# Optimization experiments

Hardware: AMD Instinct MI355X
Metric: run time of the kernel (lower is better)

## Reference

```python
import jax, jax.numpy as jnp
import numpy as np

NH, HD = 4, 16          # num_heads, head_dim (proj_dim = 64)
SCALE = HD ** -0.5
EPS = 1e-5
G = 16                  # GroupNorm groups = min(16, channels)


def _conv1x1(W, b, x):
    # 1x1 conv == channel-mixing matmul: W (out,in), x (B,in,H,W)
    return jnp.einsum('pc,bchw->bphw', W, x) + b[None, :, None, None]


def _attend(Wq, bq, Wk, bk, Wv, bv, Wo, bo, query, context):
    B, C, H, Wd = query.shape
    N = H * Wd
    q = _conv1x1(Wq, bq, query).astype(jnp.float32).reshape(B, NH, HD, N)
    k = _conv1x1(Wk, bk, context).astype(jnp.float32).reshape(B, NH, HD, N)
    v = _conv1x1(Wv, bv, context).astype(jnp.float32).reshape(B, NH, HD, N)
    attn = jax.nn.softmax(jnp.einsum('bhdn,bhdm->bhnm', q, k) * SCALE, axis=-1)
    out = jnp.einsum('bhdm,bhnm->bhdn', v, attn).reshape(B, NH * HD, H, Wd)
    return _conv1x1(Wo, bo, out)


def _gn(x, gamma, beta):
    B, C, H, W = x.shape
    xr = x.reshape(B, G, C // G, H, W)
    m = xr.mean(axis=(2, 3, 4), keepdims=True)
    v = xr.var(axis=(2, 3, 4), keepdims=True)
    xn = ((xr - m) * jax.lax.rsqrt(v + EPS)).reshape(B, C, H, W)
    return xn * gamma[None, :, None, None] + beta[None, :, None, None]


def setup_inputs() -> dict:
    key = jax.random.key(0)
    C, P, Bn, H, W = 256, 64, 2, 64, 64
    ks = iter(jax.random.split(key, 64))
    d = {}
    for m in ['a', 'b', 'c']:
        d[f'feat_{m}'] = jax.random.normal(next(ks), (Bn, C, H, W), jnp.float32)
    for m in ['a', 'b', 'c']:
        d[f'Wq_{m}'] = 0.02 * jax.random.normal(next(ks), (P, C), jnp.float32)
        d[f'bq_{m}'] = jnp.zeros((P,), jnp.float32)
        d[f'Wk_{m}'] = 0.02 * jax.random.normal(next(ks), (P, 2 * C), jnp.float32)
        d[f'bk_{m}'] = jnp.zeros((P,), jnp.float32)
        d[f'Wv_{m}'] = 0.02 * jax.random.normal(next(ks), (P, 2 * C), jnp.float32)
        d[f'bv_{m}'] = jnp.zeros((P,), jnp.float32)
        d[f'Wo_{m}'] = 0.02 * jax.random.normal(next(ks), (C, P), jnp.float32)
        d[f'bo_{m}'] = jnp.zeros((C,), jnp.float32)
        d[f'g_{m}'] = jnp.ones((C,), jnp.float32)
        d[f'be_{m}'] = jnp.zeros((C,), jnp.float32)
    return d


def reference(feat_a, feat_b, feat_c,
              Wq_a, bq_a, Wk_a, bk_a, Wv_a, bv_a, Wo_a, bo_a, g_a, be_a,
              Wq_b, bq_b, Wk_b, bk_b, Wv_b, bv_b, Wo_b, bo_b, g_b, be_b,
              Wq_c, bq_c, Wk_c, bk_c, Wv_c, bv_c, Wo_c, bo_c, g_c, be_c):
    bc = jnp.concatenate([feat_b, feat_c], axis=1)
    a_out = _gn(feat_a + _attend(Wq_a, bq_a, Wk_a, bk_a, Wv_a, bv_a, Wo_a, bo_a, feat_a, bc), g_a, be_a)
    ac = jnp.concatenate([feat_a, feat_c], axis=1)
    b_out = _gn(feat_b + _attend(Wq_b, bq_b, Wk_b, bk_b, Wv_b, bv_b, Wo_b, bo_b, feat_b, ac), g_b, be_b)
    ab = jnp.concatenate([feat_a, feat_b], axis=1)
    c_out = _gn(feat_c + _attend(Wq_c, bq_c, Wk_c, bk_c, Wv_c, bv_c, Wo_c, bo_c, feat_c, ab), g_c, be_c)
    return (a_out, b_out, c_out)
```

## Files before the change

kernel.cpp:

```cpp
#include <hip/hip_runtime.h>

#define B_ 2
#define C_ 256
#define P_ 64
#define N_ 4096
#define EPS_ 1e-5f
#define QSCALE1024_ 369.32993046757467f

typedef _Float16 half4 __attribute__((ext_vector_type(4)));
typedef _Float16 half8 __attribute__((ext_vector_type(8)));
typedef float f32x4 __attribute__((ext_vector_type(4)));
typedef float f32x16 __attribute__((ext_vector_type(16)));
typedef unsigned int uint4v __attribute__((ext_vector_type(4)));

static __device__ __forceinline__ unsigned int pkexp2(float t0, float t1) {
  unsigned int pk, tmp;
  asm("v_cvt_u32_f32 %0, %2\n\t"
      "v_cvt_u32_f32 %1, %3\n\t"
      "v_cvt_pk_u16_u32 %0, %0, %1"
      : "=&v"(pk), "=&v"(tmp)
      : "v"(t0), "v"(t1));
  return pk;
}

struct TP {
  const float* feat[3];
  const float* Wq[3]; const float* bq[3];
  const float* Wk[3]; const float* bk[3];
  const float* Wv[3]; const float* bv[3];
  const float* Wo[3]; const float* bo[3];
  const float* gm[3]; const float* bt[3];
  _Float16* q16;
  _Float16* k16;
  _Float16* v16;
  _Float16* ao0;
  _Float16* ao1;
  float* L;
  float* stats;
  float* out;
  int ctx0[3]; int ctx1[3];
};

#define PST_ 264
#define VTS_ 88

__global__ __launch_bounds__(256) void proj_fused_kernel(TP P) {
  __shared__ _Float16 bs[64 * PST_];
  const int m = blockIdx.z, b = blockIdx.y;
  const int tid = threadIdx.x;
  const int w = tid >> 6, g = (tid >> 4) & 3, t = tid & 15;
  const bool is_q = blockIdx.x >= 64;
  const int n0 = (is_q ? blockIdx.x - 64 : (int)blockIdx.x) * 64;
  const int sn = tid & 63, scb = (tid >> 6) * 16;

  if (is_q) {
    const float* __restrict__ in = P.feat[m] + (size_t)b * C_ * N_ + n0 + sn;
#pragma unroll
    for (int cc = 0; cc < 4; ++cc) {
      const int c0 = cc * 64 + scb;
      float f[16];
#pragma unroll
      for (int i = 0; i < 16; ++i) f[i] = in[(size_t)(c0 + i) * N_];
      half8 h0, h1;
#pragma unroll
      for (int j = 0; j < 8; ++j) { h0[j] = (_Float16)f[j]; h1[j] = (_Float16)f[8 + j]; }
      *(half8*)(bs + sn * PST_ + c0) = h0;
      *(half8*)(bs + sn * PST_ + c0 + 8) = h1;
    }
    __syncthreads();
    f32x4 a[4] = {{0.f,0.f,0.f,0.f},{0.f,0.f,0.f,0.f},{0.f,0.f,0.f,0.f},{0.f,0.f,0.f,0.f}};
    const float* __restrict__ Wq = P.Wq[m] + (w * 16 + t) * 256;
#pragma unroll
    for (int ks = 0; ks < 8; ++ks) {
      const float4 wa = *(const float4*)(Wq + ks * 32 + g * 8);
      const float4 wb = *(const float4*)(Wq + ks * 32 + g * 8 + 4);
      half8 af;
      af[0] = (_Float16)wa.x; af[1] = (_Float16)wa.y;
      af[2] = (_Float16)wa.z; af[3] = (_Float16)wa.w;
      af[4] = (_Float16)wb.x; af[5] = (_Float16)wb.y;
      af[6] = (_Float16)wb.z; af[7] = (_Float16)wb.w;
#pragma unroll
      for (int i = 0; i < 4; ++i) {
        const half8 bf = *(const half8*)(bs + (i * 16 + t) * PST_ + ks * 32 + g * 8);
        a[i] = __builtin_amdgcn_mfma_f32_16x16x32_f16(af, bf, a[i], 0, 0, 0);
      }
    }
    float bq[4];
#pragma unroll
    for (int r = 0; r < 4; ++r) bq[r] = P.bq[m][w * 16 + g * 4 + r];
    _Float16* qo = P.q16 + ((size_t)(m * 2 + b) * N_) * 64 + w * 16 + g * 4;
#pragma unroll
    for (int i = 0; i < 4; ++i) {
      half4 hq;
#pragma unroll
      for (int r = 0; r < 4; ++r) hq[r] = (_Float16)((a[i][r] + bq[r]) * QSCALE1024_);
      *(half4*)(qo + (size_t)(n0 + i * 16 + t) * 64) = hq;
    }
  } else {
    f32x4 ka[4] = {{0.f,0.f,0.f,0.f},{0.f,0.f,0.f,0.f},{0.f,0.f,0.f,0.f},{0.f,0.f,0.f,0.f}};
    f32x4 va[4] = {{0.f,0.f,0.f,0.f},{0.f,0.f,0.f,0.f},{0.f,0.f,0.f,0.f},{0.f,0.f,0.f,0.f}};
    const int srcs[2] = {P.ctx0[m], P.ctx1[m]};
    for (int src = 0; src < 2; ++src) {
      const float* __restrict__ in =
          P.feat[srcs[src]] + (size_t)b * C_ * N_ + n0 + sn;
      if (src) __syncthreads();
#pragma unroll
      for (int cc = 0; cc < 4; ++cc) {
        const int c0 = cc * 64 + scb;
        float f[16];
#pragma unroll
        for (int i = 0; i < 16; ++i) f[i] = in[(size_t)(c0 + i) * N_];
        half8 h0, h1;
#pragma unroll
        for (int j = 0; j < 8; ++j) { h0[j] = (_Float16)f[j]; h1[j] = (_Float16)f[8 + j]; }
        *(half8*)(bs + sn * PST_ + c0) = h0;
        *(half8*)(bs + sn * PST_ + c0 + 8) = h1;
      }
      __syncthreads();
      const float* __restrict__ Wk = P.Wk[m] + (w * 16 + t) * 512 + src * 256;
      const float* __restrict__ Wv = P.Wv[m] + (w * 16 + t) * 512 + src * 256;
#pragma unroll
      for (int ks = 0; ks < 8; ++ks) {
        const float4 k0 = *(const float4*)(Wk + ks * 32 + g * 8);
        const float4 k1 = *(const float4*)(Wk + ks * 32 + g * 8 + 4);
        const float4 v0 = *(const float4*)(Wv + ks * 32 + g * 8);
        const float4 v1 = *(const float4*)(Wv + ks * 32 + g * 8 + 4);
        half8 ak, av;
        ak[0] = (_Float16)k0.x; ak[1] = (_Float16)k0.y;
        ak[2] = (_Float16)k0.z; ak[3] = (_Float16)k0.w;
        ak[4] = (_Float16)k1.x; ak[5] = (_Float16)k1.y;
        ak[6] = (_Float16)k1.z; ak[7] = (_Float16)k1.w;
        av[0] = (_Float16)v0.x; av[1] = (_Float16)v0.y;
        av[2] = (_Float16)v0.z; av[3] = (_Float16)v0.w;
        av[4] = (_Float16)v1.x; av[5] = (_Float16)v1.y;
        av[6] = (_Float16)v1.z; av[7] = (_Float16)v1.w;
#pragma unroll
        for (int i = 0; i < 4; ++i) {
          const half8 bf = *(const half8*)(bs + (i * 16 + t) * PST_ + ks * 32 + g * 8);
          ka[i] = __builtin_amdgcn_mfma_f32_16x16x32_f16(ak, bf, ka[i], 0, 0, 0);
          va[i] = __builtin_amdgcn_mfma_f32_16x16x32_f16(av, bf, va[i], 0, 0, 0);
        }
      }
    }
    float bk[4], bv[4];
#pragma unroll
    for (int r = 0; r < 4; ++r) {
      bk[r] = P.bk[m][w * 16 + g * 4 + r];
      bv[r] = P.bv[m][w * 16 + g * 4 + r];
    }
    _Float16* ko = P.k16 + ((size_t)(m * 8 + b * 4 + w) * N_) * 16 + g * 4;
#pragma unroll
    for (int i = 0; i < 4; ++i) {
      half4 hk;
#pragma unroll
      for (int r = 0; r < 4; ++r) hk[r] = (_Float16)(ka[i][r] + bk[r]);
      *(half4*)(ko + (size_t)(n0 + i * 16 + t) * 16) = hk;
    }
    __syncthreads();
#pragma unroll
    for (int i = 0; i < 4; ++i)
#pragma unroll
      for (int r = 0; r < 4; ++r)
        bs[(w * 16 + g * 4 + r) * VTS_ + i * 16 + t] = (_Float16)(va[i][r] + bv[r]);
    __syncthreads();
#pragma unroll
    for (int pass = 0; pass < 2; ++pass) {
      const int row = pass * 32 + (tid >> 3);
      const int hh = row >> 4, dd = row & 15, nb = (tid & 7) * 8;
      const half8 hv = *(const half8*)(bs + row * VTS_ + nb);
      *(half8*)(P.v16 + ((size_t)(m * 8 + b * 4 + hh) * 16 + dd) * N_ + n0 + nb) = hv;
    }
  }
}

#define KST_ 24
#define VST_ 264

__global__ __launch_bounds__(512) void attn_kernel(TP P) {
  const int m = blockIdx.z, bh = blockIdx.y;
  const int tid = threadIdx.x;
  if (m == 0 && bh == 0 && blockIdx.x == 0 && tid < 192) P.stats[tid] = 0.f;
  const int kvh = blockIdx.x & 1, qb = blockIdx.x >> 1;
  const int kvbase = kvh * 2048;
  const int w = tid >> 6;
  const int lane = tid & 63;
  const int n = lane & 31;
  const int hh = lane >> 5;
  const int b = bh >> 2, h = bh & 3;
  const _Float16* __restrict__ kh = P.k16 + ((size_t)(m * 8 + bh) * N_) * 16;
  const _Float16* __restrict__ vh = P.v16 + ((size_t)(m * 8 + bh) * 16) * N_;
  const int q0 = qb * 256 + w * 32;
  const half8 qf = *(const half8*)(P.q16 +
      ((size_t)(m * 2 + b) * N_ + q0 + n) * 64 + h * 16 + hh * 8);

  __shared__ _Float16 ks[256 * KST_];
  __shared__ _Float16 vs[32 * VST_];

  if (tid < 32) {
    half8 o8;
#pragma unroll
    for (int j = 0; j < 8; ++j) o8[j] = (_Float16)1.0f;
    *(half8*)(vs + 16 * VST_ + tid * 8) = o8;
  }

  const int kr = tid >> 1, kc8 = tid & 1;
  const int vr = tid >> 5, vc = tid & 31;
  const _Float16* kgp = kh + (size_t)(kvbase + kr) * 16 + kc8 * 8;
  const _Float16* vgp = vh + (size_t)vr * N_ + kvbase + vc * 8;
  _Float16* ksp = ks + kr * KST_ + kc8 * 8;
  _Float16* vsp = vs + vr * VST_ + vc * 8;

  half8 kpre = *(const half8*)kgp;
  half8 vpre = *(const half8*)vgp;

  f32x16 Z, Oe, Oo;
#pragma unroll
  for (int r = 0; r < 16; ++r) { Z[r] = 15360.5f; Oe[r] = 0.f; Oo[r] = 0.f; }

  for (int c0 = 0; c0 < 2048; c0 += 256) {
    *(half8*)ksp = kpre;
    *(half8*)vsp = vpre;
    __syncthreads();
    const int nxt = (c0 + 256 < 2048) ? c0 + 256 : 0;
    kpre = *(const half8*)(kgp + (size_t)nxt * 16);
    vpre = *(const half8*)(vgp + nxt);
#pragma unroll
    for (int sub = 0; sub < 8; ++sub) {
      const half8 kf = *(const half8*)(ks + (sub * 32 + n) * KST_ + hh * 8);
      const f32x16 s = __builtin_amdgcn_mfma_f32_32x32x16_f16(kf, qf, Z, 0, 0, 0);
      unsigned int p0 = pkexp2(s[0], s[1]);
      unsigned int p1 = pkexp2(s[2], s[3]);
      unsigned int p2 = pkexp2(s[4], s[5]);
      unsigned int p3 = pkexp2(s[6], s[7]);
      unsigned int p4 = pkexp2(s[8], s[9]);
      unsigned int p5 = pkexp2(s[10], s[11]);
      unsigned int p6 = pkexp2(s[12], s[13]);
      unsigned int p7 = pkexp2(s[14], s[15]);
      asm("v_permlane32_swap_b32 %0, %1" : "+v"(p2), "+v"(p0));
      asm("v_permlane32_swap_b32 %0, %1" : "+v"(p3), "+v"(p1));
      asm("v_permlane32_swap_b32 %0, %1" : "+v"(p6), "+v"(p4));
      asm("v_permlane32_swap_b32 %0, %1" : "+v"(p7), "+v"(p5));
      const uint4v ua = {p0, p1, p2, p3};
      const uint4v ub = {p4, p5, p6, p7};
      const half8 ve = *(const half8*)(vs + n * VST_ + sub * 32 + hh * 8);
      const half8 vo = *(const half8*)(vs + n * VST_ + sub * 32 + 16 + hh * 8);
      Oe = __builtin_amdgcn_mfma_f32_32x32x16_f16(
          __builtin_bit_cast(half8, ua), ve, Oe, 0, 0, 0);
      Oo = __builtin_amdgcn_mfma_f32_32x32x16_f16(
          __builtin_bit_cast(half8, ub), vo, Oo, 0, 0, 0);
    }
    __syncthreads();
  }

  if (n < 16) {
    _Float16* aop = (kvh ? P.ao1 : P.ao0) +
                    ((size_t)(m * 2 + b) * N_ + q0) * 64 + h * 16 + n;
#pragma unroll
    for (int r = 0; r < 16; ++r) {
      const int qrow = (r & 3) + 8 * (r >> 2) + 4 * hh;
      aop[(size_t)qrow * 64] = (_Float16)(Oe[r] + Oo[r]);
    }
  } else if (n == 16) {
    float* Lp = P.L + ((size_t)(kvh * 3 + m) * 8 + bh) * N_ + q0;
#pragma unroll
    for (int r = 0; r < 16; ++r) {
      const int qrow = (r & 3) + 8 * (r >> 2) + 4 * hh;
      Lp[qrow] = Oe[r] + Oo[r];
    }
  }
}

#define BS_ 72

__global__ __launch_bounds__(256) void wo_resid_kernel(TP P) {
  __shared__ _Float16 as[64 * BS_];
  const int m = blockIdx.z;
  const int b = blockIdx.y >> 2, cblk = blockIdx.y & 3;
  const int n0 = blockIdx.x * 64;
  const int tid = threadIdx.x;
  const int w = tid >> 6, g = (tid >> 4) & 3, t = tid & 15;
  const int c0 = cblk * 64 + w * 16;
  const int c = c0 + t;
  const size_t aob = ((size_t)(m * 2 + b) * N_) * 64;

  const int ar = tid >> 2, ac = (tid & 3) * 16;
  const size_t off = (size_t)(n0 + ar) * 64 + ac;
  half8 s0 = *(const half8*)(P.ao0 + aob + off);
  half8 s1 = *(const half8*)(P.ao0 + aob + off + 8);
  const half8 u0 = *(const half8*)(P.ao1 + aob + off);
  const half8 u1 = *(const half8*)(P.ao1 + aob + off + 8);

  const float* __restrict__ L0 = P.L + ((size_t)m * 8 + b * 4) * N_;
  const float* __restrict__ L1 = P.L + ((size_t)(3 + m) * 8 + b * 4) * N_;
  float l0v[2][4], l1v[2][4];
#pragma unroll
  for (int kst = 0; kst < 2; ++kst) {
    const int head = kst * 2 + (g >> 1);
#pragma unroll
    for (int i = 0; i < 4; ++i) {
      const int nn = n0 + i * 16 + t;
      l0v[kst][i] = L0[(size_t)head * N_ + nn];
      l1v[kst][i] = L1[(size_t)head * N_ + nn];
    }
  }
  const float* __restrict__ Wo = P.Wo[m] + (size_t)c * 64;
  float4 wv0[2], wv1[2];
#pragma unroll
  for (int kst = 0; kst < 2; ++kst) {
    wv0[kst] = *(const float4*)(Wo + kst * 32 + g * 8);
    wv1[kst] = *(const float4*)(Wo + kst * 32 + g * 8 + 4);
  }
  const float bov = P.bo[m][c];
  const float* __restrict__ Xp =
      P.feat[m] + (size_t)b * C_ * N_ + (size_t)c * N_ + n0 + g * 4;
  float4 xv[4];
#pragma unroll
  for (int i = 0; i < 4; ++i) xv[i] = *(const float4*)(Xp + i * 16);

#pragma unroll
  for (int r = 0; r < 8; ++r) { s0[r] += u0[r]; s1[r] += u1[r]; }
  *(half8*)(as + ar * BS_ + ac) = s0;
  *(half8*)(as + ar * BS_ + ac + 8) = s1;
  __syncthreads();

  _Float16 hsv[2][4];
#pragma unroll
  for (int kst = 0; kst < 2; ++kst)
#pragma unroll
    for (int i = 0; i < 4; ++i)
      hsv[kst][i] = (_Float16)(1.0f / (l0v[kst][i] + l1v[kst][i]));

  f32x4 acc[4] = {{0.f,0.f,0.f,0.f},{0.f,0.f,0.f,0.f},{0.f,0.f,0.f,0.f},{0.f,0.f,0.f,0.f}};
#pragma unroll
  for (int kst = 0; kst < 2; ++kst) {
    half8 a;
    a[0] = (_Float16)wv0[kst].x; a[1] = (_Float16)wv0[kst].y;
    a[2] = (_Float16)wv0[kst].z; a[3] = (_Float16)wv0[kst].w;
    a[4] = (_Float16)wv1[kst].x; a[5] = (_Float16)wv1[kst].y;
    a[6] = (_Float16)wv1[kst].z; a[7] = (_Float16)wv1[kst].w;
#pragma unroll
    for (int i = 0; i < 4; ++i) {
      half8 bf = *(const half8*)(as + (i * 16 + t) * BS_ + kst * 32 + g * 8);
      const _Float16 hs = hsv[kst][i];
#pragma unroll
      for (int r = 0; r < 8; ++r) bf[r] *= hs;
      acc[i] = __builtin_amdgcn_mfma_f32_16x16x32_f16(bf, a, acc[i], 0, 0, 0);
    }
  }
  float* outp = P.out + (size_t)m * B_ * C_ * N_ + (size_t)b * C_ * N_ +
                (size_t)c * N_ + n0 + g * 4;
  float s = 0.f, s2 = 0.f;
#pragma unroll
  for (int i = 0; i < 4; ++i) {
    float4 o;
    o.x = acc[i][0] + xv[i].x + bov;
    o.y = acc[i][1] + xv[i].y + bov;
    o.z = acc[i][2] + xv[i].z + bov;
    o.w = acc[i][3] + xv[i].w + bov;
    s += (o.x + o.y) + (o.z + o.w);
    s2 += (o.x * o.x + o.y * o.y) + (o.z * o.z + o.w * o.w);
    *(float4*)(outp + i * 16) = o;
  }
#pragma unroll
  for (int offd = 1; offd < 64; offd <<= 1) {
    s += __shfl_xor(s, offd);
    s2 += __shfl_xor(s2, offd);
  }
  if ((tid & 63) == 0) {
    const int group = cblk * 4 + w;
    float* st = P.stats + ((size_t)(m * 2 + b) * 16 + group) * 2;
    atomicAdd(st, s);
    atomicAdd(st + 1, s2);
  }
}

__global__ __launch_bounds__(256) void gn_final_kernel(TP P) {
  const size_t idx = ((size_t)blockIdx.x * 256 + threadIdx.x) * 4;
  const int m = (int)(idx >> 21);
  const int rem = (int)(idx & ((1u << 21) - 1));
  const int b = rem >> 20;
  const int c = (rem >> 12) & 255;
  const float* st = P.stats + ((size_t)(m * 2 + b) * 16 + (c >> 4)) * 2;
  const float s0 = st[0];
  const float s1 = st[1];
  float4 x = *(float4*)(P.out + idx);
  const float mean = s0 * (1.f / 65536.f);
  const float var = s1 * (1.f / 65536.f) - mean * mean;
  const float rstd = rsqrtf(var + EPS_);
  const float ga = P.gm[m][c] * rstd, be = P.bt[m][c];
  x.x = (x.x - mean) * ga + be;
  x.y = (x.y - mean) * ga + be;
  x.z = (x.z - mean) * ga + be;
  x.w = (x.w - mean) * ga + be;
  *(float4*)(P.out + idx) = x;
}

extern "C" void kernel_launch(void* const* d_in, const int* in_sizes, int n_in,
                              void* d_out, int out_size, void* d_ws, size_t ws_size,
                              hipStream_t stream) {
  TP P;
  for (int m = 0; m < 3; ++m) {
    P.feat[m] = (const float*)d_in[m];
    const int base = 3 + m * 10;
    P.Wq[m] = (const float*)d_in[base + 0];
    P.bq[m] = (const float*)d_in[base + 1];
    P.Wk[m] = (const float*)d_in[base + 2];
    P.bk[m] = (const float*)d_in[base + 3];
    P.Wv[m] = (const float*)d_in[base + 4];
    P.bv[m] = (const float*)d_in[base + 5];
    P.Wo[m] = (const float*)d_in[base + 6];
    P.bo[m] = (const float*)d_in[base + 7];
    P.gm[m] = (const float*)d_in[base + 8];
    P.bt[m] = (const float*)d_in[base + 9];
  }
  _Float16* ws = (_Float16*)d_ws;
  P.q16 = ws;
  P.k16 = ws + 1572864;
  P.v16 = ws + 3145728;
  P.ao0 = ws + 4718592;
  P.ao1 = ws + 6291456;
  P.L = (float*)(ws + 7864320);
  P.stats = (float*)(ws + 7864320) + 196608;
  P.out = (float*)d_out;
  P.ctx0[0] = 1; P.ctx1[0] = 2;
  P.ctx0[1] = 0; P.ctx1[1] = 2;
  P.ctx0[2] = 0; P.ctx1[2] = 1;

  proj_fused_kernel<<<dim3(128, 2, 3), dim3(256), 0, stream>>>(P);
  attn_kernel<<<dim3(32, 8, 3), dim3(512), 0, stream>>>(P);
  wo_resid_kernel<<<dim3(64, 8, 3), dim3(256), 0, stream>>>(P);
  gn_final_kernel<<<dim3(6144), dim3(256), 0, stream>>>(P);
}
```

Before: 263.6 us.

## Fuse GroupNorm into Wo/residual kernel via grid-wide per-group spin barrier

Merges the separate GroupNorm pass into the Wo-projection and residual kernel. Each wavefront publishes its partial sums, bumps a per-group arrival counter and spins until all 64 contributors have arrived. It then normalizes its register-held outputs and writes them once. This removes a full read-modify-write pass over the fp32 output and one kernel launch. The cost is a spin-wait that relies on all 1536 blocks being co-resident, which is why launch bounds now request 6 blocks per SM; if they cannot all be resident the kernel could deadlock.

```diff
diff --git a/kernel.cpp b/kernel.cpp
--- a/kernel.cpp
+++ b/kernel.cpp
@@ -37,6 +37,7 @@
   _Float16* ao1;
   float* L;
   float* stats;
+  unsigned int* cnt;
   float* out;
   int ctx0[3]; int ctx1[3];
 };
@@ -179,7 +180,7 @@
 __global__ __launch_bounds__(512) void attn_kernel(TP P) {
   const int m = blockIdx.z, bh = blockIdx.y;
   const int tid = threadIdx.x;
-  if (m == 0 && bh == 0 && blockIdx.x == 0 && tid < 192) P.stats[tid] = 0.f;
+  if (m == 0 && bh == 0 && blockIdx.x == 0 && tid < 288) P.stats[tid] = 0.f;
   const int kvh = blockIdx.x & 1, qb = blockIdx.x >> 1;
   const int kvbase = kvh * 2048;
   const int w = tid >> 6;
@@ -272,7 +273,7 @@
 
 #define BS_ 72
 
-__global__ __launch_bounds__(256) void wo_resid_kernel(TP P) {
+__global__ __launch_bounds__(256, 6) void wo_gn_kernel(TP P) {
   __shared__ _Float16 as[64 * BS_];
   const int m = blockIdx.z;
   const int b = blockIdx.y >> 2, cblk = blockIdx.y & 3;
@@ -347,52 +348,55 @@
       acc[i] = __builtin_amdgcn_mfma_f32_16x16x32_f16(bf, a, acc[i], 0, 0, 0);
     }
   }
-  float* outp = P.out + (size_t)m * B_ * C_ * N_ + (size_t)b * C_ * N_ +
-                (size_t)c * N_ + n0 + g * 4;
+  float4 ov[4];
   float s = 0.f, s2 = 0.f;
 #pragma unroll
   for (int i = 0; i < 4; ++i) {
-    float4 o;
-    o.x = acc[i][0] + xv[i].x + bov;
-    o.y = acc[i][1] + xv[i].y + bov;
-    o.z = acc[i][2] + xv[i].z + bov;
-    o.w = acc[i][3] + xv[i].w + bov;
-    s += (o.x + o.y) + (o.z + o.w);
-    s2 += (o.x * o.x + o.y * o.y) + (o.z * o.z + o.w * o.w);
-    *(float4*)(outp + i * 16) = o;
+    ov[i].x = acc[i][0] + xv[i].x + bov;
+    ov[i].y = acc[i][1] + xv[i].y + bov;
+    ov[i].z = acc[i][2] + xv[i].z + bov;
+    ov[i].w = acc[i][3] + xv[i].w + bov;
+    s += (ov[i].x + ov[i].y) + (ov[i].z + ov[i].w);
+    s2 += (ov[i].x * ov[i].x + ov[i].y * ov[i].y) +
+          (ov[i].z * ov[i].z + ov[i].w * ov[i].w);
   }
 #pragma unroll
   for (int offd = 1; offd < 64; offd <<= 1) {
     s += __shfl_xor(s, offd);
     s2 += __shfl_xor(s2, offd);
   }
+  const int group = cblk * 4 + w;
+  float* st = P.stats + ((size_t)(m * 2 + b) * 16 + group) * 2;
+  unsigned int* cp = P.cnt + (size_t)(m * 2 + b) * 16 + group;
+
+  float sm = 0.f, sq = 0.f;
   if ((tid & 63) == 0) {
-    const int group = cblk * 4 + w;
-    float* st = P.stats + ((size_t)(m * 2 + b) * 16 + group) * 2;
     atomicAdd(st, s);
     atomicAdd(st + 1, s2);
-  }
-}
-
-__global__ __launch_bounds__(256) void gn_final_kernel(TP P) {
-  const size_t idx = ((size_t)blockIdx.x * 256 + threadIdx.x) * 4;
-  const int m = (int)(idx >> 21);
-  const int rem = (int)(idx & ((1u << 21) - 1));
-  const int b = rem >> 20;
-  const int c = (rem >> 12) & 255;
-  const float* st = P.stats + ((size_t)(m * 2 + b) * 16 + (c >> 4)) * 2;
-  const float s0 = st[0];
-  const float s1 = st[1];
-  float4 x = *(float4*)(P.out + idx);
-  const float mean = s0 * (1.f / 65536.f);
-  const float var = s1 * (1.f / 65536.f) - mean * mean;
+    __hip_atomic_fetch_add(cp, 1u, __ATOMIC_RELEASE, __HIP_MEMORY_SCOPE_AGENT);
+    while (__hip_atomic_load(cp, __ATOMIC_ACQUIRE, __HIP_MEMORY_SCOPE_AGENT) < 64u)
+      __builtin_amdgcn_s_sleep(2);
+    sm = __hip_atomic_load(st + 0, __ATOMIC_RELAXED, __HIP_MEMORY_SCOPE_AGENT);
+    sq = __hip_atomic_load(st + 1, __ATOMIC_RELAXED, __HIP_MEMORY_SCOPE_AGENT);
+  }
+  sm = __shfl(sm, 0);
+  sq = __shfl(sq, 0);
+
+  const float mean = sm * (1.f / 65536.f);
+  const float var = sq * (1.f / 65536.f) - mean * mean;
   const float rstd = rsqrtf(var + EPS_);
   const float ga = P.gm[m][c] * rstd, be = P.bt[m][c];
-  x.x = (x.x - mean) * ga + be;
-  x.y = (x.y - mean) * ga + be;
-  x.z = (x.z - mean) * ga + be;
-  x.w = (x.w - mean) * ga + be;
-  *(float4*)(P.out + idx) = x;
+  float* outp = P.out + (size_t)m * B_ * C_ * N_ + (size_t)b * C_ * N_ +
+                (size_t)c * N_ + n0 + g * 4;
+#pragma unroll
+  for (int i = 0; i < 4; ++i) {
+    float4 o;
+    o.x = (ov[i].x - mean) * ga + be;
+    o.y = (ov[i].y - mean) * ga + be;
+    o.z = (ov[i].z - mean) * ga + be;
+    o.w = (ov[i].w - mean) * ga + be;
+    *(float4*)(outp + i * 16) = o;
+  }
 }
 
 extern "C" void kernel_launch(void* const* d_in, const int* in_sizes, int n_in,
@@ -421,6 +425,7 @@
   P.ao1 = ws + 6291456;
   P.L = (float*)(ws + 7864320);
   P.stats = (float*)(ws + 7864320) + 196608;
+  P.cnt = (unsigned int*)(P.stats + 192);
   P.out = (float*)d_out;
   P.ctx0[0] = 1; P.ctx1[0] = 2;
   P.ctx0[1] = 0; P.ctx1[1] = 2;
@@ -428,6 +433,5 @@
 
   proj_fused_kernel<<<dim3(128, 2, 3), dim3(256), 0, stream>>>(P);
   attn_kernel<<<dim3(32, 8, 3), dim3(512), 0, stream>>>(P);
-  wo_resid_kernel<<<dim3(64, 8, 3), dim3(256), 0, stream>>>(P);
-  gn_final_kernel<<<dim3(6144), dim3(256), 0, stream>>>(P);
+  wo_gn_kernel<<<dim3(64, 8, 3), dim3(256), 0, stream>>>(P);
 }
```

Result: slower. 740.0 us (+180.8%).
